# Performance work log

Measured on AMD Instinct MI355X. Metric: run time of the kernel, lower is better.

Reference implementation:

```python
import jax, jax.numpy as jnp
import numpy as np


def setup_inputs() -> dict:
    key = jax.random.key(0)
    k1, k2, k3, k4 = jax.random.split(key, 4)
    B, Q, K, H, D = 2, 2048, 2048, 16, 64
    qs = jax.random.normal(k1, (B, Q, H, D), dtype=jnp.float32)
    ks = jax.random.normal(k2, (B, K, H, D), dtype=jnp.float32)
    vs = jax.random.normal(k3, (B, K, H, D), dtype=jnp.float32)
    # valid lengths in [1, K] so no row is fully masked
    valid_lens = jnp.maximum(jax.random.randint(k4, (B,), 0, K + 1, dtype=jnp.int32), 1)
    return {"qs": qs, "ks": ks, "vs": vs, "valid_lens": valid_lens}


def reference(qs, ks, vs, valid_lens):
    # Faithful math of ScanAttention: scaled dot-product attention with a
    # per-batch key-validity mask (online-softmax scan == exact softmax).
    B, Q, H, D = qs.shape
    K = ks.shape[1]
    scale = 1.0 / jnp.sqrt(jnp.float32(D))
    # [B, H, Q, K]
    scores = jnp.einsum('bqhd,bkhd->bhqk', qs * scale, ks)
    ks_mask = jnp.arange(K)[None, :] < valid_lens[:, None]  # [B, K]
    scores = jnp.where(ks_mask[:, None, None, :], scores, -jnp.inf)
    attn = jax.nn.softmax(scores, axis=-1)
    out = jnp.einsum('bhqk,bkhd->bqhd', attn, vs)  # [B, Q, H, D]
    return out
```

## Files before the change

kernel.cpp:

```cpp
#include <hip/hip_runtime.h>
#include <hip/hip_bf16.h>

typedef __bf16 bf16t;
typedef bf16t bf16x8 __attribute__((ext_vector_type(8)));
typedef float f32x4 __attribute__((ext_vector_type(4)));
typedef float f32x16 __attribute__((ext_vector_type(16)));
typedef unsigned short u16x8 __attribute__((ext_vector_type(8)));
typedef unsigned int u32x4 __attribute__((ext_vector_type(4)));

#define NB 2
#define NQ 2048
#define NK 2048
#define NH 16
#define ND 64
#define HD (NH * ND)
#define KVBLK 64
#define SCALE_LOG2E 0.18033688011112042f
#define RESCALE_THR 8.0f

__device__ inline unsigned cvt_pk_bf16(float a, float b) {
    unsigned r;
    asm("v_cvt_pk_bf16_f32 %0, %1, %2" : "=v"(r) : "v"(a), "v"(b));
    return r;
}

__device__ inline void plswap(unsigned& a, unsigned& b) {
#if __has_builtin(__builtin_amdgcn_permlane32_swap)
    auto r = __builtin_amdgcn_permlane32_swap(a, b, false, false);
    a = r[0]; b = r[1];
#else
    const unsigned as = __shfl_xor((int)a, 32);
    const unsigned bs = __shfl_xor((int)b, 32);
    const bool hi = (threadIdx.x & 32) != 0;
    const unsigned na = hi ? bs : a;
    const unsigned nb = hi ? b : as;
    a = na; b = nb;
#endif
}

__global__ __launch_bounds__(256)
void scan_attn(const float* __restrict__ qs, const float* __restrict__ ks,
               const float* __restrict__ vs, const int* __restrict__ vlen,
               float* __restrict__ out)
{
    const int bid  = blockIdx.x;
    const int b    = bid & 1;
    const int h    = (bid >> 1) & 15;
    const int qt   = bid >> 5;
    const int tid  = threadIdx.x;
    const int wid  = tid >> 6;
    const int lane = tid & 63;
    const int ql   = lane & 31;
    const int hi   = lane >> 5;
    const int swq  = (ql & 7) << 4;
    const int q    = qt * 128 + wid * 32 + ql;

    const int nkv    = vlen[b];
    const int ntiles = (nkv + KVBLK - 1) >> 6;
    const int rem    = nkv & 63;

    const float* qptr = qs + ((size_t)b * NQ + q) * HD + h * ND;
    const float* kptr = ks + (size_t)b * NK * HD + h * ND;
    const float* vptr = vs + (size_t)b * NK * HD + h * ND;

    __shared__ __align__(16) char k_lds[2][KVBLK * 64 * 2];
    __shared__ __align__(16) char vt_lds[2][64 * KVBLK * 2];

    bf16x8 qf[4];
#pragma unroll
    for (int c = 0; c < 4; ++c) {
        const float* p = qptr + 16 * c + 8 * hi;
        f32x4 lo = *reinterpret_cast<const f32x4*>(p);
        f32x4 h4 = *reinterpret_cast<const f32x4*>(p + 4);
#pragma unroll
        for (int j = 0; j < 4; ++j) {
            qf[c][j]     = (bf16t)(lo[j] * SCALE_LOG2E);
            qf[c][4 + j] = (bf16t)(h4[j] * SCALE_LOG2E);
        }
    }

    const int skr  = tid >> 2;
    const int skc2 = (tid & 3) << 5;
    const int ksw  = (skr & 7) << 4;
    const int svd  = tid & 63;
    const int svk2 = (tid >> 6) << 5;
    const int vsw  = (svd & 7) << 4;

    f32x4 kreg[4];
    float vreg[16];

    auto load_tile = [&](int kb) {
        const float* kp = kptr + (size_t)(kb + skr) * HD + ((tid & 3) << 4);
#pragma unroll
        for (int i = 0; i < 4; ++i)
            kreg[i] = *reinterpret_cast<const f32x4*>(kp + 4 * i);
        const float* vp = vptr + (size_t)(kb + ((tid >> 6) << 4)) * HD + svd;
#pragma unroll
        for (int j = 0; j < 16; ++j)
            vreg[j] = vp[(size_t)j * HD];
    };

    auto store_tile = [&](int buf) {
        u16x8 w0, w1;
#pragma unroll
        for (int i = 0; i < 4; ++i)
#pragma unroll
            for (int j = 0; j < 4; ++j) {
                const int e = 4 * i + j;
                const unsigned short u =
                    __builtin_bit_cast(unsigned short, (bf16t)kreg[i][j]);
                if (e < 8) w0[e] = u; else w1[e - 8] = u;
            }
        char* kb_ = k_lds[buf] + skr * 128;
        *reinterpret_cast<u16x8*>(kb_ + (skc2 ^ ksw))        = w0;
        *reinterpret_cast<u16x8*>(kb_ + ((skc2 + 16) ^ ksw)) = w1;

        u16x8 x0, x1;
#pragma unroll
        for (int j = 0; j < 16; ++j) {
            const unsigned short u =
                __builtin_bit_cast(unsigned short, (bf16t)vreg[j]);
            if (j < 8) x0[j] = u; else x1[j - 8] = u;
        }
        char* vb_ = vt_lds[buf] + svd * 128;
        *reinterpret_cast<u16x8*>(vb_ + (svk2 ^ vsw))        = x0;
        *reinterpret_cast<u16x8*>(vb_ + ((svk2 + 16) ^ vsw)) = x1;
    };

    float mrun = -__builtin_inff();
    float lrun = 0.0f;
    f32x16 o[2] = {};

    load_tile(0);
    store_tile(0);
    __syncthreads();

    int cur = 0;
    for (int t = 0; t < ntiles; ++t) {
        const int kb = t << 6;
        const bool has_next = (t + 1) < ntiles;
        if (has_next) load_tile(kb + KVBLK);

        const char* kbuf = k_lds[cur];
        f32x16 s[2];
#pragma unroll
        for (int h2 = 0; h2 < 2; ++h2) {
            f32x16 acc = {};
            const char* krow = kbuf + (32 * h2 + ql) * 128;
#pragma unroll
            for (int c = 0; c < 4; ++c) {
                bf16x8 kf = *reinterpret_cast<const bf16x8*>(
                    krow + ((32 * c + 16 * hi) ^ swq));
                acc = __builtin_amdgcn_mfma_f32_32x32x16_bf16(kf, qf[c], acc, 0, 0, 0);
            }
            s[h2] = acc;
        }

        if (rem && t == ntiles - 1) {
            const int krem = nkv - kb;
#pragma unroll
            for (int h2 = 0; h2 < 2; ++h2)
#pragma unroll
                for (int r = 0; r < 16; ++r)
                    if (32 * h2 + (r & 3) + 8 * (r >> 2) + 4 * hi >= krem)
                        s[h2][r] = -__builtin_inff();
        }

        float pmax = -__builtin_inff();
#pragma unroll
        for (int h2 = 0; h2 < 2; ++h2)
#pragma unroll
            for (int r = 0; r < 16; ++r) pmax = fmaxf(pmax, s[h2][r]);
        pmax = fmaxf(pmax, __shfl_xor(pmax, 32));

        if (!__all(pmax <= mrun + RESCALE_THR)) {
            const float mnew  = fmaxf(mrun, pmax);
            const float alpha = exp2f(mrun - mnew);
            lrun *= alpha;
            o[0] *= alpha;
            o[1] *= alpha;
            mrun = mnew;
        }

        float ps = 0.0f;
#pragma unroll
        for (int h2 = 0; h2 < 2; ++h2)
#pragma unroll
            for (int r = 0; r < 16; ++r) {
                const float pv = exp2f(s[h2][r] - mrun);
                s[h2][r] = pv;
                ps += pv;
            }
        ps += __shfl_xor(ps, 32);
        lrun += ps;

        bf16x8 pf[4];
#pragma unroll
        for (int c = 0; c < 4; ++c) {
            const int h2 = c >> 1, r0 = (c & 1) * 8;
            unsigned a0 = cvt_pk_bf16(s[h2][r0 + 0], s[h2][r0 + 1]);
            unsigned b0 = cvt_pk_bf16(s[h2][r0 + 4], s[h2][r0 + 5]);
            plswap(a0, b0);
            unsigned a1 = cvt_pk_bf16(s[h2][r0 + 2], s[h2][r0 + 3]);
            unsigned b1 = cvt_pk_bf16(s[h2][r0 + 6], s[h2][r0 + 7]);
            plswap(a1, b1);
            pf[c] = __builtin_bit_cast(bf16x8, (u32x4){a0, a1, b0, b1});
        }

        const char* vbuf = vt_lds[cur];
#pragma unroll
        for (int dt = 0; dt < 2; ++dt) {
            const char* vrow = vbuf + (32 * dt + ql) * 128;
#pragma unroll
            for (int c = 0; c < 4; ++c) {
                bf16x8 vf = *reinterpret_cast<const bf16x8*>(
                    vrow + ((32 * c + 16 * hi) ^ swq));
                o[dt] = __builtin_amdgcn_mfma_f32_32x32x16_bf16(vf, pf[c], o[dt], 0, 0, 0);
            }
        }

        if (has_next) store_tile(cur ^ 1);
        __syncthreads();
        cur ^= 1;
    }

    const float inv = 1.0f / lrun;
    float* op = out + ((size_t)b * NQ + q) * HD + h * ND;
#pragma unroll
    for (int dt = 0; dt < 2; ++dt)
#pragma unroll
        for (int rg = 0; rg < 4; ++rg) {
            f32x4 w;
#pragma unroll
            for (int e = 0; e < 4; ++e) w[e] = o[dt][4 * rg + e] * inv;
            *reinterpret_cast<f32x4*>(op + 32 * dt + 8 * rg + 4 * hi) = w;
        }
}

extern "C" void kernel_launch(void* const* d_in, const int* in_sizes, int n_in,
                              void* d_out, int out_size, void* d_ws, size_t ws_size,
                              hipStream_t stream)
{
    const float* qs   = (const float*)d_in[0];
    const float* ks   = (const float*)d_in[1];
    const float* vs   = (const float*)d_in[2];
    const int*   vlen = (const int*)d_in[3];
    float* out = (float*)d_out;

    dim3 grid(NB * NH * (NQ / 128));
    dim3 block(256);
    scan_attn<<<grid, block, 0, stream>>>(qs, ks, vs, vlen, out);
}
```

Baseline: 61.44 us.

## Split KV sequence across four wave groups per block with LDS merge

Raises the block to 1024 threads: four groups of four waves each process an interleaved quarter of the KV tiles for the same 128 queries. Each group keeps its own double-buffered K/V LDS staging, and at the end the partial (max, sum, output) states are combined through LDS using an online-softmax merge. The block index is also remapped so that consecutive blocks interleave heads and batches differently. This aims to shorten the serial KV loop per block and raise wave-level parallelism. In exchange it uses 128KB+ of LDS, limits occupancy to one block per CU, and adds a reduction step plus idle groups when the number of tiles is small.

Measured after the change: 101.2 us. 64.8% more time.

```diff
diff --git a/kernel.cpp b/kernel.cpp
--- a/kernel.cpp
+++ b/kernel.cpp
@@ -3,6 +3,7 @@
 
 typedef __bf16 bf16t;
 typedef bf16t bf16x8 __attribute__((ext_vector_type(8)));
+typedef float f32x2 __attribute__((ext_vector_type(2)));
 typedef float f32x4 __attribute__((ext_vector_type(4)));
 typedef float f32x16 __attribute__((ext_vector_type(16)));
 typedef unsigned short u16x8 __attribute__((ext_vector_type(8)));
@@ -38,33 +39,40 @@
 #endif
 }
 
-__global__ __launch_bounds__(256)
+__global__ __launch_bounds__(1024)
 void scan_attn(const float* __restrict__ qs, const float* __restrict__ ks,
                const float* __restrict__ vs, const int* __restrict__ vlen,
                float* __restrict__ out)
 {
-    const int bid  = blockIdx.x;
-    const int b    = bid & 1;
-    const int h    = (bid >> 1) & 15;
-    const int qt   = bid >> 5;
+    const int bid = blockIdx.x;
+    const int x   = bid & 7;
+    const int j   = bid >> 3;
+    const int b   = j & 1;
+    const int idx = x | ((j >> 1) << 3);
+    const int h   = idx & 15;
+    const int qt  = idx >> 4;
+
     const int tid  = threadIdx.x;
     const int wid  = tid >> 6;
+    const int g3   = wid >> 2;
+    const int wq   = wid & 3;
     const int lane = tid & 63;
     const int ql   = lane & 31;
     const int hi   = lane >> 5;
     const int swq  = (ql & 7) << 4;
-    const int q    = qt * 128 + wid * 32 + ql;
+    const int gtid = tid & 255;
+    const int q    = qt * 128 + wq * 32 + ql;
 
     const int nkv    = vlen[b];
     const int ntiles = (nkv + KVBLK - 1) >> 6;
     const int rem    = nkv & 63;
+    const int tmax   = (ntiles + 3) >> 2;
 
     const float* qptr = qs + ((size_t)b * NQ + q) * HD + h * ND;
     const float* kptr = ks + (size_t)b * NK * HD + h * ND;
     const float* vptr = vs + (size_t)b * NK * HD + h * ND;
 
-    __shared__ __align__(16) char k_lds[2][KVBLK * 64 * 2];
-    __shared__ __align__(16) char vt_lds[2][64 * KVBLK * 2];
+    __shared__ __align__(16) char smem[4][2][16384];
 
     bf16x8 qf[4];
 #pragma unroll
@@ -73,31 +81,31 @@
         f32x4 lo = *reinterpret_cast<const f32x4*>(p);
         f32x4 h4 = *reinterpret_cast<const f32x4*>(p + 4);
 #pragma unroll
-        for (int j = 0; j < 4; ++j) {
-            qf[c][j]     = (bf16t)(lo[j] * SCALE_LOG2E);
-            qf[c][4 + j] = (bf16t)(h4[j] * SCALE_LOG2E);
+        for (int jj = 0; jj < 4; ++jj) {
+            qf[c][jj]     = (bf16t)(lo[jj] * SCALE_LOG2E);
+            qf[c][4 + jj] = (bf16t)(h4[jj] * SCALE_LOG2E);
         }
     }
 
-    const int skr  = tid >> 2;
-    const int skc2 = (tid & 3) << 5;
+    const int skr  = gtid >> 2;
+    const int skc2 = (gtid & 3) << 5;
     const int ksw  = (skr & 7) << 4;
-    const int svd  = tid & 63;
-    const int svk2 = (tid >> 6) << 5;
+    const int svd  = gtid & 63;
+    const int svk2 = (gtid >> 6) << 5;
     const int vsw  = (svd & 7) << 4;
 
     f32x4 kreg[4];
     float vreg[16];
 
     auto load_tile = [&](int kb) {
-        const float* kp = kptr + (size_t)(kb + skr) * HD + ((tid & 3) << 4);
+        const float* kp = kptr + (size_t)(kb + skr) * HD + ((gtid & 3) << 4);
 #pragma unroll
         for (int i = 0; i < 4; ++i)
             kreg[i] = *reinterpret_cast<const f32x4*>(kp + 4 * i);
-        const float* vp = vptr + (size_t)(kb + ((tid >> 6) << 4)) * HD + svd;
-#pragma unroll
-        for (int j = 0; j < 16; ++j)
-            vreg[j] = vp[(size_t)j * HD];
+        const float* vp = vptr + (size_t)(kb + ((gtid >> 6) << 4)) * HD + svd;
+#pragma unroll
+        for (int jj = 0; jj < 16; ++jj)
+            vreg[jj] = vp[(size_t)jj * HD];
     };
 
     auto store_tile = [&](int buf) {
@@ -105,24 +113,24 @@
 #pragma unroll
         for (int i = 0; i < 4; ++i)
 #pragma unroll
-            for (int j = 0; j < 4; ++j) {
-                const int e = 4 * i + j;
+            for (int jj = 0; jj < 4; ++jj) {
+                const int e = 4 * i + jj;
                 const unsigned short u =
-                    __builtin_bit_cast(unsigned short, (bf16t)kreg[i][j]);
+                    __builtin_bit_cast(unsigned short, (bf16t)kreg[i][jj]);
                 if (e < 8) w0[e] = u; else w1[e - 8] = u;
             }
-        char* kb_ = k_lds[buf] + skr * 128;
+        char* kb_ = smem[g3][buf] + skr * 128;
         *reinterpret_cast<u16x8*>(kb_ + (skc2 ^ ksw))        = w0;
         *reinterpret_cast<u16x8*>(kb_ + ((skc2 + 16) ^ ksw)) = w1;
 
         u16x8 x0, x1;
 #pragma unroll
-        for (int j = 0; j < 16; ++j) {
+        for (int jj = 0; jj < 16; ++jj) {
             const unsigned short u =
-                __builtin_bit_cast(unsigned short, (bf16t)vreg[j]);
-            if (j < 8) x0[j] = u; else x1[j - 8] = u;
-        }
-        char* vb_ = vt_lds[buf] + svd * 128;
+                __builtin_bit_cast(unsigned short, (bf16t)vreg[jj]);
+            if (jj < 8) x0[jj] = u; else x1[jj - 8] = u;
+        }
+        char* vb_ = smem[g3][buf] + 8192 + svd * 128;
         *reinterpret_cast<u16x8*>(vb_ + (svk2 ^ vsw))        = x0;
         *reinterpret_cast<u16x8*>(vb_ + ((svk2 + 16) ^ vsw)) = x1;
     };
@@ -131,91 +139,94 @@
     float lrun = 0.0f;
     f32x16 o[2] = {};
 
-    load_tile(0);
-    store_tile(0);
+    if (g3 < ntiles) { load_tile(g3 << 6); store_tile(0); }
     __syncthreads();
 
     int cur = 0;
-    for (int t = 0; t < ntiles; ++t) {
-        const int kb = t << 6;
-        const bool has_next = (t + 1) < ntiles;
-        if (has_next) load_tile(kb + KVBLK);
-
-        const char* kbuf = k_lds[cur];
-        f32x16 s[2];
-#pragma unroll
-        for (int h2 = 0; h2 < 2; ++h2) {
-            f32x16 acc = {};
-            const char* krow = kbuf + (32 * h2 + ql) * 128;
+    for (int i = 0; i < tmax; ++i) {
+        const int tile = 4 * i + g3;
+        const bool active   = tile < ntiles;
+        const bool has_next = tile + 4 < ntiles;
+        if (has_next) load_tile((tile + 4) << 6);
+
+        if (active) {
+            const int kb = tile << 6;
+            const char* kbuf = smem[g3][cur];
+            f32x16 s[2];
+#pragma unroll
+            for (int h2 = 0; h2 < 2; ++h2) {
+                f32x16 acc = {};
+                const char* krow = kbuf + (32 * h2 + ql) * 128;
+#pragma unroll
+                for (int c = 0; c < 4; ++c) {
+                    bf16x8 kf = *reinterpret_cast<const bf16x8*>(
+                        krow + ((32 * c + 16 * hi) ^ swq));
+                    acc = __builtin_amdgcn_mfma_f32_32x32x16_bf16(kf, qf[c], acc, 0, 0, 0);
+                }
+                s[h2] = acc;
+            }
+
+            if (rem && tile == ntiles - 1) {
+                const int krem = nkv - kb;
+#pragma unroll
+                for (int h2 = 0; h2 < 2; ++h2)
+#pragma unroll
+                    for (int r = 0; r < 16; ++r)
+                        if (32 * h2 + (r & 3) + 8 * (r >> 2) + 4 * hi >= krem)
+                            s[h2][r] = -__builtin_inff();
+            }
+
+            float pmax = -__builtin_inff();
+#pragma unroll
+            for (int h2 = 0; h2 < 2; ++h2)
+#pragma unroll
+                for (int r = 0; r < 16; ++r) pmax = fmaxf(pmax, s[h2][r]);
+            pmax = fmaxf(pmax, __shfl_xor(pmax, 32));
+
+            if (!__all(pmax <= mrun + RESCALE_THR)) {
+                const float mnew  = fmaxf(mrun, pmax);
+                const float alpha = exp2f(mrun - mnew);
+                lrun *= alpha;
+                o[0] *= alpha;
+                o[1] *= alpha;
+                mrun = mnew;
+            }
+
+            float ps = 0.0f;
+#pragma unroll
+            for (int h2 = 0; h2 < 2; ++h2)
+#pragma unroll
+                for (int r = 0; r < 16; ++r) {
+                    const float pv = exp2f(s[h2][r] - mrun);
+                    s[h2][r] = pv;
+                    ps += pv;
+                }
+            ps += __shfl_xor(ps, 32);
+            lrun += ps;
+
+            bf16x8 pf[4];
 #pragma unroll
             for (int c = 0; c < 4; ++c) {
-                bf16x8 kf = *reinterpret_cast<const bf16x8*>(
-                    krow + ((32 * c + 16 * hi) ^ swq));
-                acc = __builtin_amdgcn_mfma_f32_32x32x16_bf16(kf, qf[c], acc, 0, 0, 0);
-            }
-            s[h2] = acc;
-        }
-
-        if (rem && t == ntiles - 1) {
-            const int krem = nkv - kb;
-#pragma unroll
-            for (int h2 = 0; h2 < 2; ++h2)
-#pragma unroll
-                for (int r = 0; r < 16; ++r)
-                    if (32 * h2 + (r & 3) + 8 * (r >> 2) + 4 * hi >= krem)
-                        s[h2][r] = -__builtin_inff();
-        }
-
-        float pmax = -__builtin_inff();
-#pragma unroll
-        for (int h2 = 0; h2 < 2; ++h2)
-#pragma unroll
-            for (int r = 0; r < 16; ++r) pmax = fmaxf(pmax, s[h2][r]);
-        pmax = fmaxf(pmax, __shfl_xor(pmax, 32));
-
-        if (!__all(pmax <= mrun + RESCALE_THR)) {
-            const float mnew  = fmaxf(mrun, pmax);
-            const float alpha = exp2f(mrun - mnew);
-            lrun *= alpha;
-            o[0] *= alpha;
-            o[1] *= alpha;
-            mrun = mnew;
-        }
-
-        float ps = 0.0f;
-#pragma unroll
-        for (int h2 = 0; h2 < 2; ++h2)
-#pragma unroll
-            for (int r = 0; r < 16; ++r) {
-                const float pv = exp2f(s[h2][r] - mrun);
-                s[h2][r] = pv;
-                ps += pv;
-            }
-        ps += __shfl_xor(ps, 32);
-        lrun += ps;
-
-        bf16x8 pf[4];
-#pragma unroll
-        for (int c = 0; c < 4; ++c) {
-            const int h2 = c >> 1, r0 = (c & 1) * 8;
-            unsigned a0 = cvt_pk_bf16(s[h2][r0 + 0], s[h2][r0 + 1]);
-            unsigned b0 = cvt_pk_bf16(s[h2][r0 + 4], s[h2][r0 + 5]);
-            plswap(a0, b0);
-            unsigned a1 = cvt_pk_bf16(s[h2][r0 + 2], s[h2][r0 + 3]);
-            unsigned b1 = cvt_pk_bf16(s[h2][r0 + 6], s[h2][r0 + 7]);
-            plswap(a1, b1);
-            pf[c] = __builtin_bit_cast(bf16x8, (u32x4){a0, a1, b0, b1});
-        }
-
-        const char* vbuf = vt_lds[cur];
-#pragma unroll
-        for (int dt = 0; dt < 2; ++dt) {
-            const char* vrow = vbuf + (32 * dt + ql) * 128;
-#pragma unroll
-            for (int c = 0; c < 4; ++c) {
-                bf16x8 vf = *reinterpret_cast<const bf16x8*>(
-                    vrow + ((32 * c + 16 * hi) ^ swq));
-                o[dt] = __builtin_amdgcn_mfma_f32_32x32x16_bf16(vf, pf[c], o[dt], 0, 0, 0);
+                const int h2 = c >> 1, r0 = (c & 1) * 8;
+                unsigned a0 = cvt_pk_bf16(s[h2][r0 + 0], s[h2][r0 + 1]);
+                unsigned b0 = cvt_pk_bf16(s[h2][r0 + 4], s[h2][r0 + 5]);
+                plswap(a0, b0);
+                unsigned a1 = cvt_pk_bf16(s[h2][r0 + 2], s[h2][r0 + 3]);
+                unsigned b1 = cvt_pk_bf16(s[h2][r0 + 6], s[h2][r0 + 7]);
+                plswap(a1, b1);
+                pf[c] = __builtin_bit_cast(bf16x8, (u32x4){a0, a1, b0, b1});
+            }
+
+            const char* vbuf = smem[g3][cur] + 8192;
+#pragma unroll
+            for (int dt = 0; dt < 2; ++dt) {
+                const char* vrow = vbuf + (32 * dt + ql) * 128;
+#pragma unroll
+                for (int c = 0; c < 4; ++c) {
+                    bf16x8 vf = *reinterpret_cast<const bf16x8*>(
+                        vrow + ((32 * c + 16 * hi) ^ swq));
+                    o[dt] = __builtin_amdgcn_mfma_f32_32x32x16_bf16(vf, pf[c], o[dt], 0, 0, 0);
+                }
             }
         }
 
@@ -224,17 +235,63 @@
         cur ^= 1;
     }
 
-    const float inv = 1.0f / lrun;
-    float* op = out + ((size_t)b * NQ + q) * HD + h * ND;
-#pragma unroll
-    for (int dt = 0; dt < 2; ++dt)
-#pragma unroll
-        for (int rg = 0; rg < 4; ++rg) {
-            f32x4 w;
-#pragma unroll
-            for (int e = 0; e < 4; ++e) w[e] = o[dt][4 * rg + e] * inv;
-            *reinterpret_cast<f32x4*>(op + 32 * dt + 8 * rg + 4 * hi) = w;
-        }
+    {
+        char*  mo_base = &smem[0][0][0];
+        f32x2* ml      = (f32x2*)(mo_base + 98304);
+        const int swl  = (lane & 7) << 4;
+
+        if (g3 > 0) {
+            const int sidx = ((g3 - 1) * 4 + wq) * 64 + lane;
+            char* so = mo_base + sidx * 128;
+#pragma unroll
+            for (int c = 0; c < 8; ++c) {
+                f32x4 w;
+#pragma unroll
+                for (int e = 0; e < 4; ++e)
+                    w[e] = (c < 4) ? o[0][4 * c + e] : o[1][4 * (c - 4) + e];
+                *reinterpret_cast<f32x4*>(so + ((16 * c) ^ swl)) = w;
+            }
+            ml[sidx] = (f32x2){mrun, lrun};
+        }
+        __syncthreads();
+
+        if (g3 == 0) {
+            f32x2 mg[3];
+            float M = mrun;
+#pragma unroll
+            for (int g = 0; g < 3; ++g) {
+                mg[g] = ml[(g * 4 + wq) * 64 + lane];
+                M = fmaxf(M, mg[g][0]);
+            }
+            const float ws = exp2f(mrun - M);
+            float lsum = lrun * ws;
+            float wg[3];
+#pragma unroll
+            for (int g = 0; g < 3; ++g) {
+                wg[g] = exp2f(mg[g][0] - M);
+                lsum += mg[g][1] * wg[g];
+            }
+            const float inv = 1.0f / lsum;
+
+            float* op = out + ((size_t)b * NQ + q) * HD + h * ND;
+#pragma unroll
+            for (int c = 0; c < 8; ++c) {
+                f32x4 acc;
+#pragma unroll
+                for (int e = 0; e < 4; ++e)
+                    acc[e] = ((c < 4) ? o[0][4 * c + e] : o[1][4 * (c - 4) + e]) * ws;
+#pragma unroll
+                for (int g = 0; g < 3; ++g) {
+                    f32x4 w = *reinterpret_cast<const f32x4*>(
+                        mo_base + ((g * 4 + wq) * 64 + lane) * 128 + ((16 * c) ^ swl));
+                    acc += wg[g] * w;
+                }
+                const int dt = c >> 2, rg = c & 3;
+                f32x4 res = acc * inv;
+                *reinterpret_cast<f32x4*>(op + 32 * dt + 8 * rg + 4 * hi) = res;
+            }
+        }
+    }
 }
 
 extern "C" void kernel_launch(void* const* d_in, const int* in_sizes, int n_in,
@@ -248,6 +305,6 @@
     float* out = (float*)d_out;
 
     dim3 grid(NB * NH * (NQ / 128));
-    dim3 block(256);
+    dim3 block(1024);
     scan_attn<<<grid, block, 0, stream>>>(qs, ks, vs, vlen, out);
 }
```

## Split KV sequence across blocks and merge partial attention outputs

Applied to the files above, without the earlier changes.

Adds a flash-decoding style split of each query tile's KV range into 2 or 4 chunks processed by separate blocks. Each block writes unnormalized bf16 partial outputs plus running max and sum to workspace, and a second merge kernel combines them with softmax rescaling. The block index is also remapped so that batch varies across consecutive groups, spreading the uneven valid lengths. This raises the block count from 512 to as many as 2048 to fill the GPU's CUs. The cost is an extra launch, workspace traffic, and bf16 rounding of the partials.

New measurement: 85.59 us. 1.39x slower.

```diff
diff --git a/kernel.cpp b/kernel.cpp
--- a/kernel.cpp
+++ b/kernel.cpp
@@ -2,7 +2,9 @@
 #include <hip/hip_bf16.h>
 
 typedef __bf16 bf16t;
+typedef bf16t bf16x4 __attribute__((ext_vector_type(4)));
 typedef bf16t bf16x8 __attribute__((ext_vector_type(8)));
+typedef float f32x2 __attribute__((ext_vector_type(2)));
 typedef float f32x4 __attribute__((ext_vector_type(4)));
 typedef float f32x16 __attribute__((ext_vector_type(16)));
 typedef unsigned short u16x8 __attribute__((ext_vector_type(8)));
@@ -15,8 +17,12 @@
 #define ND 64
 #define HD (NH * ND)
 #define KVBLK 64
+#define NUNITS 512
 #define SCALE_LOG2E 0.18033688011112042f
 #define RESCALE_THR 8.0f
+
+#define OPART_BYTES(n) ((size_t)(n) * 8388608ULL)
+#define ML_BYTES(n)    ((size_t)(n) * 524288ULL)
 
 __device__ inline unsigned cvt_pk_bf16(float a, float b) {
     unsigned r;
@@ -31,51 +37,60 @@
 #else
     const unsigned as = __shfl_xor((int)a, 32);
     const unsigned bs = __shfl_xor((int)b, 32);
-    const bool hi = (threadIdx.x & 32) != 0;
-    const unsigned na = hi ? bs : a;
-    const unsigned nb = hi ? b : as;
+    const bool lh = (threadIdx.x & 32) != 0;
+    const unsigned na = lh ? bs : a;
+    const unsigned nb = lh ? b : as;
     a = na; b = nb;
 #endif
 }
 
+template <int NSPLIT>
 __global__ __launch_bounds__(256)
 void scan_attn(const float* __restrict__ qs, const float* __restrict__ ks,
                const float* __restrict__ vs, const int* __restrict__ vlen,
-               float* __restrict__ out)
+               float* __restrict__ out, char* __restrict__ ws)
 {
-    const int bid  = blockIdx.x;
-    const int b    = bid & 1;
-    const int h    = (bid >> 1) & 15;
-    const int qt   = bid >> 5;
+    const int bid = blockIdx.x;
+    const int x    = bid & 7;
+    const int jj   = bid >> 3;
+    const int b    = jj & 1;
+    const int code = x | ((jj >> 1) << 3);
+    const int qt   = code / (16 * NSPLIT);
+    const int rr   = code % (16 * NSPLIT);
+    const int h    = rr / NSPLIT;
+    const int s    = rr % NSPLIT;
+    const int uidx = ((b * NH + h) << 4) + qt;
+
     const int tid  = threadIdx.x;
-    const int wid  = tid >> 6;
+    const int wq   = tid >> 6;
     const int lane = tid & 63;
     const int ql   = lane & 31;
-    const int hi   = lane >> 5;
+    const int lh   = lane >> 5;
     const int swq  = (ql & 7) << 4;
-    const int q    = qt * 128 + wid * 32 + ql;
+    const int q    = qt * 128 + wq * 32 + ql;
 
     const int nkv    = vlen[b];
     const int ntiles = (nkv + KVBLK - 1) >> 6;
     const int rem    = nkv & 63;
+    const int tlo    = (ntiles * s) / NSPLIT;
+    const int thi    = (ntiles * (s + 1)) / NSPLIT;
 
     const float* qptr = qs + ((size_t)b * NQ + q) * HD + h * ND;
     const float* kptr = ks + (size_t)b * NK * HD + h * ND;
     const float* vptr = vs + (size_t)b * NK * HD + h * ND;
 
-    __shared__ __align__(16) char k_lds[2][KVBLK * 64 * 2];
-    __shared__ __align__(16) char vt_lds[2][64 * KVBLK * 2];
+    __shared__ __align__(16) char smem[2][16384];
 
     bf16x8 qf[4];
 #pragma unroll
     for (int c = 0; c < 4; ++c) {
-        const float* p = qptr + 16 * c + 8 * hi;
-        f32x4 lo = *reinterpret_cast<const f32x4*>(p);
-        f32x4 h4 = *reinterpret_cast<const f32x4*>(p + 4);
-#pragma unroll
-        for (int j = 0; j < 4; ++j) {
-            qf[c][j]     = (bf16t)(lo[j] * SCALE_LOG2E);
-            qf[c][4 + j] = (bf16t)(h4[j] * SCALE_LOG2E);
+        const float* p = qptr + 16 * c + 8 * lh;
+        f32x4 lo4 = *reinterpret_cast<const f32x4*>(p);
+        f32x4 hi4 = *reinterpret_cast<const f32x4*>(p + 4);
+#pragma unroll
+        for (int e = 0; e < 4; ++e) {
+            qf[c][e]     = (bf16t)(lo4[e] * SCALE_LOG2E);
+            qf[c][4 + e] = (bf16t)(hi4[e] * SCALE_LOG2E);
         }
     }
 
@@ -96,8 +111,8 @@
             kreg[i] = *reinterpret_cast<const f32x4*>(kp + 4 * i);
         const float* vp = vptr + (size_t)(kb + ((tid >> 6) << 4)) * HD + svd;
 #pragma unroll
-        for (int j = 0; j < 16; ++j)
-            vreg[j] = vp[(size_t)j * HD];
+        for (int e = 0; e < 16; ++e)
+            vreg[e] = vp[(size_t)e * HD];
     };
 
     auto store_tile = [&](int buf) {
@@ -105,24 +120,24 @@
 #pragma unroll
         for (int i = 0; i < 4; ++i)
 #pragma unroll
-            for (int j = 0; j < 4; ++j) {
-                const int e = 4 * i + j;
+            for (int e = 0; e < 4; ++e) {
+                const int el = 4 * i + e;
                 const unsigned short u =
-                    __builtin_bit_cast(unsigned short, (bf16t)kreg[i][j]);
-                if (e < 8) w0[e] = u; else w1[e - 8] = u;
-            }
-        char* kb_ = k_lds[buf] + skr * 128;
+                    __builtin_bit_cast(unsigned short, (bf16t)kreg[i][e]);
+                if (el < 8) w0[el] = u; else w1[el - 8] = u;
+            }
+        char* kb_ = smem[buf] + skr * 128;
         *reinterpret_cast<u16x8*>(kb_ + (skc2 ^ ksw))        = w0;
         *reinterpret_cast<u16x8*>(kb_ + ((skc2 + 16) ^ ksw)) = w1;
 
         u16x8 x0, x1;
 #pragma unroll
-        for (int j = 0; j < 16; ++j) {
+        for (int e = 0; e < 16; ++e) {
             const unsigned short u =
-                __builtin_bit_cast(unsigned short, (bf16t)vreg[j]);
-            if (j < 8) x0[j] = u; else x1[j - 8] = u;
-        }
-        char* vb_ = vt_lds[buf] + svd * 128;
+                __builtin_bit_cast(unsigned short, (bf16t)vreg[e]);
+            if (e < 8) x0[e] = u; else x1[e - 8] = u;
+        }
+        char* vb_ = smem[buf] + 8192 + svd * 128;
         *reinterpret_cast<u16x8*>(vb_ + (svk2 ^ vsw))        = x0;
         *reinterpret_cast<u16x8*>(vb_ + ((svk2 + 16) ^ vsw)) = x1;
     };
@@ -131,18 +146,17 @@
     float lrun = 0.0f;
     f32x16 o[2] = {};
 
-    load_tile(0);
-    store_tile(0);
+    if (tlo < thi) { load_tile(tlo << 6); store_tile(0); }
     __syncthreads();
 
     int cur = 0;
-    for (int t = 0; t < ntiles; ++t) {
+    for (int t = tlo; t < thi; ++t) {
         const int kb = t << 6;
-        const bool has_next = (t + 1) < ntiles;
-        if (has_next) load_tile(kb + KVBLK);
-
-        const char* kbuf = k_lds[cur];
-        f32x16 s[2];
+        const bool has_next = (t + 1) < thi;
+        if (has_next) load_tile((t + 1) << 6);
+
+        const char* kbuf = smem[cur];
+        f32x16 s_[2];
 #pragma unroll
         for (int h2 = 0; h2 < 2; ++h2) {
             f32x16 acc = {};
@@ -150,10 +164,10 @@
 #pragma unroll
             for (int c = 0; c < 4; ++c) {
                 bf16x8 kf = *reinterpret_cast<const bf16x8*>(
-                    krow + ((32 * c + 16 * hi) ^ swq));
+                    krow + ((32 * c + 16 * lh) ^ swq));
                 acc = __builtin_amdgcn_mfma_f32_32x32x16_bf16(kf, qf[c], acc, 0, 0, 0);
             }
-            s[h2] = acc;
+            s_[h2] = acc;
         }
 
         if (rem && t == ntiles - 1) {
@@ -162,15 +176,15 @@
             for (int h2 = 0; h2 < 2; ++h2)
 #pragma unroll
                 for (int r = 0; r < 16; ++r)
-                    if (32 * h2 + (r & 3) + 8 * (r >> 2) + 4 * hi >= krem)
-                        s[h2][r] = -__builtin_inff();
+                    if (32 * h2 + (r & 3) + 8 * (r >> 2) + 4 * lh >= krem)
+                        s_[h2][r] = -__builtin_inff();
         }
 
         float pmax = -__builtin_inff();
 #pragma unroll
         for (int h2 = 0; h2 < 2; ++h2)
 #pragma unroll
-            for (int r = 0; r < 16; ++r) pmax = fmaxf(pmax, s[h2][r]);
+            for (int r = 0; r < 16; ++r) pmax = fmaxf(pmax, s_[h2][r]);
         pmax = fmaxf(pmax, __shfl_xor(pmax, 32));
 
         if (!__all(pmax <= mrun + RESCALE_THR)) {
@@ -187,8 +201,8 @@
         for (int h2 = 0; h2 < 2; ++h2)
 #pragma unroll
             for (int r = 0; r < 16; ++r) {
-                const float pv = exp2f(s[h2][r] - mrun);
-                s[h2][r] = pv;
+                const float pv = exp2f(s_[h2][r] - mrun);
+                s_[h2][r] = pv;
                 ps += pv;
             }
         ps += __shfl_xor(ps, 32);
@@ -198,23 +212,23 @@
 #pragma unroll
         for (int c = 0; c < 4; ++c) {
             const int h2 = c >> 1, r0 = (c & 1) * 8;
-            unsigned a0 = cvt_pk_bf16(s[h2][r0 + 0], s[h2][r0 + 1]);
-            unsigned b0 = cvt_pk_bf16(s[h2][r0 + 4], s[h2][r0 + 5]);
+            unsigned a0 = cvt_pk_bf16(s_[h2][r0 + 0], s_[h2][r0 + 1]);
+            unsigned b0 = cvt_pk_bf16(s_[h2][r0 + 4], s_[h2][r0 + 5]);
             plswap(a0, b0);
-            unsigned a1 = cvt_pk_bf16(s[h2][r0 + 2], s[h2][r0 + 3]);
-            unsigned b1 = cvt_pk_bf16(s[h2][r0 + 6], s[h2][r0 + 7]);
+            unsigned a1 = cvt_pk_bf16(s_[h2][r0 + 2], s_[h2][r0 + 3]);
+            unsigned b1 = cvt_pk_bf16(s_[h2][r0 + 6], s_[h2][r0 + 7]);
             plswap(a1, b1);
             pf[c] = __builtin_bit_cast(bf16x8, (u32x4){a0, a1, b0, b1});
         }
 
-        const char* vbuf = vt_lds[cur];
+        const char* vbuf = smem[cur] + 8192;
 #pragma unroll
         for (int dt = 0; dt < 2; ++dt) {
             const char* vrow = vbuf + (32 * dt + ql) * 128;
 #pragma unroll
             for (int c = 0; c < 4; ++c) {
                 bf16x8 vf = *reinterpret_cast<const bf16x8*>(
-                    vrow + ((32 * c + 16 * hi) ^ swq));
+                    vrow + ((32 * c + 16 * lh) ^ swq));
                 o[dt] = __builtin_amdgcn_mfma_f32_32x32x16_bf16(vf, pf[c], o[dt], 0, 0, 0);
             }
         }
@@ -224,17 +238,91 @@
         cur ^= 1;
     }
 
-    const float inv = 1.0f / lrun;
-    float* op = out + ((size_t)b * NQ + q) * HD + h * ND;
-#pragma unroll
-    for (int dt = 0; dt < 2; ++dt)
-#pragma unroll
-        for (int rg = 0; rg < 4; ++rg) {
-            f32x4 w;
-#pragma unroll
-            for (int e = 0; e < 4; ++e) w[e] = o[dt][4 * rg + e] * inv;
-            *reinterpret_cast<f32x4*>(op + 32 * dt + 8 * rg + 4 * hi) = w;
-        }
+    if (NSPLIT == 1) {
+        const float inv = 1.0f / lrun;
+        float* op = out + ((size_t)b * NQ + q) * HD + h * ND;
+#pragma unroll
+        for (int dt = 0; dt < 2; ++dt)
+#pragma unroll
+            for (int rg = 0; rg < 4; ++rg) {
+                f32x4 w;
+#pragma unroll
+                for (int e = 0; e < 4; ++e) w[e] = o[dt][4 * rg + e] * inv;
+                *reinterpret_cast<f32x4*>(op + 32 * dt + 8 * rg + 4 * lh) = w;
+            }
+    } else {
+        const int p = uidx * NSPLIT + s;
+        bf16t* op = (bf16t*)ws + ((size_t)p * 128 + wq * 32 + ql) * 64;
+#pragma unroll
+        for (int dt = 0; dt < 2; ++dt)
+#pragma unroll
+            for (int rg = 0; rg < 4; ++rg) {
+                bf16x4 w;
+#pragma unroll
+                for (int e = 0; e < 4; ++e) w[e] = (bf16t)o[dt][4 * rg + e];
+                *reinterpret_cast<bf16x4*>(op + 32 * dt + 8 * rg + 4 * lh) = w;
+            }
+        if (lh == 0) {
+            f32x2* ml = (f32x2*)(ws + OPART_BYTES(NSPLIT));
+            ml[p * 128 + wq * 32 + ql] = (f32x2){mrun, lrun};
+        }
+    }
+}
+
+template <int NSPLIT>
+__global__ __launch_bounds__(256)
+void merge_attn(const char* __restrict__ ws, float* __restrict__ out)
+{
+    const int u  = blockIdx.x;
+    const int b  = u >> 8;
+    const int h  = (u >> 4) & 15;
+    const int qt = u & 15;
+    const int tid = threadIdx.x;
+    const int q  = tid >> 1;
+    const int dh = (tid & 1) * 32;
+
+    const bf16t* opart = (const bf16t*)ws;
+    const f32x2* ml    = (const f32x2*)(ws + OPART_BYTES(NSPLIT));
+
+    float m_s[NSPLIT], l_s[NSPLIT];
+    float M = -__builtin_inff();
+#pragma unroll
+    for (int s = 0; s < NSPLIT; ++s) {
+        f32x2 v = ml[(u * NSPLIT + s) * 128 + q];
+        m_s[s] = v[0]; l_s[s] = v[1];
+        M = fmaxf(M, v[0]);
+    }
+    float L = 0.0f, w_s[NSPLIT];
+#pragma unroll
+    for (int s = 0; s < NSPLIT; ++s) {
+        w_s[s] = exp2f(m_s[s] - M);
+        L += w_s[s] * l_s[s];
+    }
+    const float inv = 1.0f / L;
+
+    float acc[32];
+#pragma unroll
+    for (int e = 0; e < 32; ++e) acc[e] = 0.0f;
+#pragma unroll
+    for (int s = 0; s < NSPLIT; ++s) {
+        const bf16t* op = opart + ((size_t)(u * NSPLIT + s) * 128 + q) * 64 + dh;
+#pragma unroll
+        for (int c = 0; c < 4; ++c) {
+            bf16x8 v8 = *reinterpret_cast<const bf16x8*>(op + 8 * c);
+#pragma unroll
+            for (int e = 0; e < 8; ++e)
+                acc[8 * c + e] += w_s[s] * (float)v8[e];
+        }
+    }
+
+    float* op = out + ((size_t)b * NQ + qt * 128 + q) * HD + h * ND + dh;
+#pragma unroll
+    for (int c = 0; c < 8; ++c) {
+        f32x4 st;
+#pragma unroll
+        for (int e = 0; e < 4; ++e) st[e] = acc[4 * c + e] * inv;
+        *reinterpret_cast<f32x4*>(op + 4 * c) = st;
+    }
 }
 
 extern "C" void kernel_launch(void* const* d_in, const int* in_sizes, int n_in,
@@ -246,8 +334,18 @@
     const float* vs   = (const float*)d_in[2];
     const int*   vlen = (const int*)d_in[3];
     float* out = (float*)d_out;
-
-    dim3 grid(NB * NH * (NQ / 128));
-    dim3 block(256);
-    scan_attn<<<grid, block, 0, stream>>>(qs, ks, vs, vlen, out);
-}
+    char*  ws  = (char*)d_ws;
+
+    const size_t need4 = OPART_BYTES(4) + ML_BYTES(4);
+    const size_t need2 = OPART_BYTES(2) + ML_BYTES(2);
+
+    if (ws_size >= need4) {
+        scan_attn<4><<<NUNITS * 4, 256, 0, stream>>>(qs, ks, vs, vlen, out, ws);
+        merge_attn<4><<<NUNITS, 256, 0, stream>>>(ws, out);
+    } else if (ws_size >= need2) {
+        scan_attn<2><<<NUNITS * 2, 256, 0, stream>>>(qs, ks, vs, vlen, out, ws);
+        merge_attn<2><<<NUNITS, 256, 0, stream>>>(ws, out);
+    } else {
+        scan_attn<1><<<NUNITS, 256, 0, stream>>>(qs, ks, vs, vlen, out, ws);
+    }
+}
```
